# Kernel optimization log

Hardware: AMD Instinct MI355X
Metric: run time of the kernel (lower is better)

## Reference

```python
import jax, jax.numpy as jnp
import numpy as np

N = 8192

def setup_inputs() -> dict:
    key = jax.random.key(0)
    k1, k2, k3, k4, k5, k6 = jax.random.split(key, 6)
    return {
        "t": jnp.zeros((), dtype=jnp.float32),
        "state": jax.random.uniform(k1, (3 * N,), dtype=jnp.float32),
        "betas": jax.random.uniform(k2, (N,), dtype=jnp.float32),
        "deltas": jax.random.uniform(k3, (N,), dtype=jnp.float32),
        "cs": jax.random.uniform(k4, (N,), dtype=jnp.float32),
        "ps": jax.random.uniform(k5, (N,), dtype=jnp.float32),
        "ts": jax.random.uniform(k6, (N, N), dtype=jnp.float32) * 0.5,
    }

def reference(t, state, betas, deltas, cs, ps, ts):
    # squared parametrization of all learned params
    T = jnp.square(ts)                      # [N, N]
    diag = jnp.diagonal(T)                  # T[n, n]
    row_sum = jnp.sum(T, axis=1)            # sum over T[n, :]
    # normalization[n] = min(T[n,n] / (sum_k T[n,k] - T[n,n]), 1)
    norm = jnp.minimum(diag / (row_sum - diag), jnp.float32(1.0))

    s = state.reshape(-1, 3)                # [N, 3] -> (U, I, V) per host
    U, I, V = s[:, 0], s[:, 1], s[:, 2]

    b2 = jnp.square(betas)
    d2 = jnp.square(deltas)
    p2 = jnp.square(ps)
    c2 = jnp.square(cs)

    bUV = b2 * U * V
    dU = -bUV
    dI = bUV - d2 * I
    # coupling[n] = sum_{nbr != n} norm[nbr] * T[nbr, n] * V[nbr]
    coupling = (norm * V) @ T - norm * diag * V
    dV = p2 * I - c2 * V - diag + coupling

    return jnp.stack([dU, dI, dV], axis=1).reshape(-1)
```

## Files before the change

### kernel.cpp

```cpp
#include <hip/hip_runtime.h>

#define NN 8192
#define RPB 8
#define NBLK (NN / RPB)
#define SLICE2 32


__global__ void __launch_bounds__(256)
main_pass(const float* __restrict__ ts,
          const float* __restrict__ state,
          float* __restrict__ wv,
          float* __restrict__ diag,
          float* __restrict__ partial)
{
    __shared__ float red[4];
    __shared__ float wbc;

    const int tid  = threadIdx.x;
    const int lane = tid & 63;
    const int wid  = tid >> 6;
    const int row0 = blockIdx.x * RPB;

    float4 acc[8];
    #pragma unroll
    for (int k = 0; k < 8; ++k) acc[k] = make_float4(0.f, 0.f, 0.f, 0.f);

    float4 cur[8], nxt[8];
    {
        const float4* rp = (const float4*)(ts + (size_t)row0 * NN);
        #pragma unroll
        for (int k = 0; k < 8; ++k) cur[k] = rp[tid + k * 256];
    }

    #pragma unroll
    for (int r = 0; r < RPB; ++r) {
        const int row = row0 + r;
        if (r + 1 < RPB) {
            const float4* np = (const float4*)(ts + (size_t)(row + 1) * NN);
            #pragma unroll
            for (int k = 0; k < 8; ++k) nxt[k] = np[tid + k * 256];
        }
        float s = 0.f;
        #pragma unroll
        for (int k = 0; k < 8; ++k) {
            float4 v = cur[k];
            s += v.x * v.x + v.y * v.y + v.z * v.z + v.w * v.w;
        }
        #pragma unroll
        for (int off = 32; off; off >>= 1) s += __shfl_down(s, off);
        if (lane == 0) red[wid] = s;
        __syncthreads();
        if (tid == 0) {
            const float total = red[0] + red[1] + red[2] + red[3];
            float d = ts[(size_t)row * NN + row];
            d *= d;
            const float nrm = fminf(d / (total - d), 1.0f);
            const float wr  = nrm * state[3 * row + 2];
            wv[row]   = wr;
            diag[row] = d;
            wbc = wr;
        }
        __syncthreads();
        const float wr = wbc;
        #pragma unroll
        for (int k = 0; k < 8; ++k) {
            float4 v = cur[k];
            acc[k].x += wr * v.x * v.x;
            acc[k].y += wr * v.y * v.y;
            acc[k].z += wr * v.z * v.z;
            acc[k].w += wr * v.w * v.w;
        }
        if (r + 1 < RPB) {
            #pragma unroll
            for (int k = 0; k < 8; ++k) cur[k] = nxt[k];
        }
    }
    float4* po = (float4*)(partial + (size_t)blockIdx.x * NN);
    #pragma unroll
    for (int k = 0; k < 8; ++k) po[tid + k * 256] = acc[k];
}

__global__ void __launch_bounds__(256)
reduce1(const float* __restrict__ partial, float* __restrict__ partial2)
{
    const int col = blockIdx.x * 1024 + threadIdx.x * 4;
    const float* base = partial + (size_t)blockIdx.y * 32 * NN + col;
    float4 acc = {0.f, 0.f, 0.f, 0.f};
    #pragma unroll 8
    for (int k = 0; k < 32; ++k) {
        float4 v = *(const float4*)(base + (size_t)k * NN);
        acc.x += v.x; acc.y += v.y; acc.z += v.z; acc.w += v.w;
    }
    *(float4*)(partial2 + (size_t)blockIdx.y * NN + col) = acc;
}

__global__ void __launch_bounds__(256)
finalize(const float* __restrict__ state,
         const float* __restrict__ betas,
         const float* __restrict__ deltas,
         const float* __restrict__ cs,
         const float* __restrict__ ps,
         const float* __restrict__ wv,
         const float* __restrict__ diag,
         const float* __restrict__ partial2,
         float* __restrict__ out)
{
    const int j = blockIdx.x * 256 + threadIdx.x;
    float coup = 0.f;
    #pragma unroll 8
    for (int k = 0; k < SLICE2; ++k) coup += partial2[(size_t)k * NN + j];
    const float dj = diag[j];
    coup -= wv[j] * dj;

    const float U = state[3 * j + 0];
    const float I = state[3 * j + 1];
    const float V = state[3 * j + 2];
    const float b2 = betas[j] * betas[j];
    const float d2 = deltas[j] * deltas[j];
    const float p2 = ps[j] * ps[j];
    const float c2 = cs[j] * cs[j];
    const float bUV = b2 * U * V;

    out[3 * j + 0] = -bUV;
    out[3 * j + 1] = bUV - d2 * I;
    out[3 * j + 2] = p2 * I - c2 * V - dj + coup;
}

extern "C" void kernel_launch(void* const* d_in, const int* in_sizes, int n_in,
                              void* d_out, int out_size, void* d_ws, size_t ws_size,
                              hipStream_t stream) {
    const float* state  = (const float*)d_in[1];
    const float* betas  = (const float*)d_in[2];
    const float* deltas = (const float*)d_in[3];
    const float* cs     = (const float*)d_in[4];
    const float* ps     = (const float*)d_in[5];
    const float* ts     = (const float*)d_in[6];
    float* out = (float*)d_out;

    float* wv       = (float*)d_ws;
    float* diag     = wv + NN;
    float* partial  = diag + NN;
    float* partial2 = partial + (size_t)NBLK * NN;

    main_pass<<<NBLK, 256, 0, stream>>>(ts, state, wv, diag, partial);
    reduce1<<<dim3(8, SLICE2), 256, 0, stream>>>(partial, partial2);
    finalize<<<NN / 256, 256, 0, stream>>>(state, betas, deltas, cs, ps,
                                           wv, diag, partial2, out);
}
```

Baseline: 380.5 us.

## Double-buffer row reduction to drop a barrier, stream ts non-temporally, double rows per block

The main pass now keeps per-row partial sums in a double-buffered shared array, so every thread computes the row total and weight itself. This removes the second barrier and the thread-0 serial section from each row. It also prefetches the diagonal and V value for the next row, loads ts with non-temporal hints, and handles 16 rows per block instead of 8. That halves the partial-sum buffer, so reduce1 now sums 16 slices instead of 32. The trade-off is fewer blocks (512) for the whole GPU and redundant per-thread scalar math.

After: 376.8 us. Within noise of the previous version (-1.0%).

```diff
diff --git a/kernel.cpp b/kernel.cpp
--- a/kernel.cpp
+++ b/kernel.cpp
@@ -1,9 +1,12 @@
 #include <hip/hip_runtime.h>
 
 #define NN 8192
-#define RPB 8
+#define RPB 16
 #define NBLK (NN / RPB)
+#define SLICE1 16
 #define SLICE2 32
+
+typedef float vf4 __attribute__((ext_vector_type(4)));
 
 
 __global__ void __launch_bounds__(256)
@@ -13,58 +16,57 @@
           float* __restrict__ diag,
           float* __restrict__ partial)
 {
-    __shared__ float red[4];
-    __shared__ float wbc;
+    __shared__ float red[2][4];
 
     const int tid  = threadIdx.x;
     const int lane = tid & 63;
     const int wid  = tid >> 6;
     const int row0 = blockIdx.x * RPB;
 
-    float4 acc[8];
+    vf4 acc[8];
     #pragma unroll
-    for (int k = 0; k < 8; ++k) acc[k] = make_float4(0.f, 0.f, 0.f, 0.f);
+    for (int k = 0; k < 8; ++k) acc[k] = (vf4)(0.f);
 
-    float4 cur[8], nxt[8];
+    vf4 cur[8], nxt[8];
     {
-        const float4* rp = (const float4*)(ts + (size_t)row0 * NN);
+        const vf4* rp = (const vf4*)(ts + (size_t)row0 * NN);
         #pragma unroll
-        for (int k = 0; k < 8; ++k) cur[k] = rp[tid + k * 256];
+        for (int k = 0; k < 8; ++k)
+            cur[k] = __builtin_nontemporal_load(rp + tid + k * 256);
     }
+    float dcur = ts[(size_t)row0 * NN + row0];
+    float vcur = state[3 * row0 + 2];
 
     #pragma unroll
     for (int r = 0; r < RPB; ++r) {
         const int row = row0 + r;
+        float dnxt = 0.f, vnxt = 0.f;
         if (r + 1 < RPB) {
-            const float4* np = (const float4*)(ts + (size_t)(row + 1) * NN);
+            const vf4* np = (const vf4*)(ts + (size_t)(row + 1) * NN);
             #pragma unroll
-            for (int k = 0; k < 8; ++k) nxt[k] = np[tid + k * 256];
+            for (int k = 0; k < 8; ++k)
+                nxt[k] = __builtin_nontemporal_load(np + tid + k * 256);
+            dnxt = ts[(size_t)(row + 1) * NN + (row + 1)];
+            vnxt = state[3 * (row + 1) + 2];
         }
         float s = 0.f;
         #pragma unroll
         for (int k = 0; k < 8; ++k) {
-            float4 v = cur[k];
+            vf4 v = cur[k];
             s += v.x * v.x + v.y * v.y + v.z * v.z + v.w * v.w;
         }
         #pragma unroll
         for (int off = 32; off; off >>= 1) s += __shfl_down(s, off);
-        if (lane == 0) red[wid] = s;
+        if (lane == 0) red[r & 1][wid] = s;
         __syncthreads();
-        if (tid == 0) {
-            const float total = red[0] + red[1] + red[2] + red[3];
-            float d = ts[(size_t)row * NN + row];
-            d *= d;
-            const float nrm = fminf(d / (total - d), 1.0f);
-            const float wr  = nrm * state[3 * row + 2];
-            wv[row]   = wr;
-            diag[row] = d;
-            wbc = wr;
-        }
-        __syncthreads();
-        const float wr = wbc;
+        const float total = red[r & 1][0] + red[r & 1][1]
+                          + red[r & 1][2] + red[r & 1][3];
+        const float d  = dcur * dcur;
+        const float wr = fminf(d / (total - d), 1.0f) * vcur;
+        if (tid == 0) { wv[row] = wr; diag[row] = d; }
         #pragma unroll
         for (int k = 0; k < 8; ++k) {
-            float4 v = cur[k];
+            vf4 v = cur[k];
             acc[k].x += wr * v.x * v.x;
             acc[k].y += wr * v.y * v.y;
             acc[k].z += wr * v.z * v.z;
@@ -73,9 +75,11 @@
         if (r + 1 < RPB) {
             #pragma unroll
             for (int k = 0; k < 8; ++k) cur[k] = nxt[k];
+            dcur = dnxt;
+            vcur = vnxt;
         }
     }
-    float4* po = (float4*)(partial + (size_t)blockIdx.x * NN);
+    vf4* po = (vf4*)(partial + (size_t)blockIdx.x * NN);
     #pragma unroll
     for (int k = 0; k < 8; ++k) po[tid + k * 256] = acc[k];
 }
@@ -84,14 +88,14 @@
 reduce1(const float* __restrict__ partial, float* __restrict__ partial2)
 {
     const int col = blockIdx.x * 1024 + threadIdx.x * 4;
-    const float* base = partial + (size_t)blockIdx.y * 32 * NN + col;
-    float4 acc = {0.f, 0.f, 0.f, 0.f};
-    #pragma unroll 8
-    for (int k = 0; k < 32; ++k) {
-        float4 v = *(const float4*)(base + (size_t)k * NN);
-        acc.x += v.x; acc.y += v.y; acc.z += v.z; acc.w += v.w;
+    const float* base = partial + (size_t)blockIdx.y * SLICE1 * NN + col;
+    vf4 acc = (vf4)(0.f);
+    #pragma unroll
+    for (int k = 0; k < SLICE1; ++k) {
+        vf4 v = *(const vf4*)(base + (size_t)k * NN);
+        acc += v;
     }
-    *(float4*)(partial2 + (size_t)blockIdx.y * NN + col) = acc;
+    *(vf4*)(partial2 + (size_t)blockIdx.y * NN + col) = acc;
 }
 
 __global__ void __launch_bounds__(256)
```
